# Kernel tuning notes

Measured on AMD Instinct MI355X. Metric: run time of the kernel, lower is better.

## Reference

```python
import jax, jax.numpy as jnp
import numpy as np

B, T, IN_DIM, HID, OUT_DIM = 64, 1024, 128, 512, 64


def _lstm_layer(x, w_ih, w_hh, b_ih, b_hh):
    """Single LSTM layer, batch_first input x: [B, T, D] -> h_seq [B, T, H].
    PyTorch gate order: i, f, g, o. h0 = c0 = 0."""
    H = w_hh.shape[1]
    # Precompute input contribution for all timesteps (one big GEMM).
    xW = jnp.einsum('btd,gd->btg', x, w_ih) + b_ih + b_hh  # [B, T, 4H]
    xW_t = jnp.swapaxes(xW, 0, 1)  # [T, B, 4H] for scan over time

    def step(carry, xw_t):
        h, c = carry
        gates = xw_t + h @ w_hh.T  # [B, 4H]
        i = jax.nn.sigmoid(gates[:, 0 * H:1 * H])
        f = jax.nn.sigmoid(gates[:, 1 * H:2 * H])
        g = jnp.tanh(gates[:, 2 * H:3 * H])
        o = jax.nn.sigmoid(gates[:, 3 * H:4 * H])
        c_new = f * c + i * g
        h_new = o * jnp.tanh(c_new)
        return (h_new, c_new), h_new

    h0 = jnp.zeros((x.shape[0], H), dtype=x.dtype)
    c0 = jnp.zeros((x.shape[0], H), dtype=x.dtype)
    _, h_seq = jax.lax.scan(step, (h0, c0), xW_t)  # h_seq: [T, B, H]
    return jnp.swapaxes(h_seq, 0, 1)  # [B, T, H]


def setup_inputs() -> dict:
    key = jax.random.key(0)
    ks = jax.random.split(key, 12)
    s0 = 1.0 / np.sqrt(HID)  # PyTorch default uniform(-1/sqrt(H), 1/sqrt(H))
    u = lambda k, shape: jax.random.uniform(k, shape, jnp.float32, -s0, s0)
    return {
        'inputs': jax.random.normal(ks[0], (B, T, IN_DIM), jnp.float32),
        # layer 0
        'w_ih_0': u(ks[1], (4 * HID, IN_DIM)),
        'w_hh_0': u(ks[2], (4 * HID, HID)),
        'b_ih_0': u(ks[3], (4 * HID,)),
        'b_hh_0': u(ks[4], (4 * HID,)),
        # layer 1
        'w_ih_1': u(ks[5], (4 * HID, HID)),
        'w_hh_1': u(ks[6], (4 * HID, HID)),
        'b_ih_1': u(ks[7], (4 * HID,)),
        'b_hh_1': u(ks[8], (4 * HID,)),
        # final linear
        'fc_w': u(ks[9], (OUT_DIM, HID)),
        'fc_b': u(ks[10], (OUT_DIM,)),
    }


def reference(inputs, w_ih_0, w_hh_0, b_ih_0, b_hh_0,
              w_ih_1, w_hh_1, b_ih_1, b_hh_1, fc_w, fc_b):
    h1 = _lstm_layer(inputs, w_ih_0, w_hh_0, b_ih_0, b_hh_0)  # [B, T, H]
    h2 = _lstm_layer(h1, w_ih_1, w_hh_1, b_ih_1, b_hh_1)      # [B, T, H]
    last = h2[:, -1, :]                                        # [B, H]
    return last @ fc_w.T + fc_b                                # [B, OUT_DIM]
```

## Files before the change

kernel.cpp:

```cpp
#include <hip/hip_runtime.h>
#include <hip/hip_bf16.h>


#define NTH 256
#define WPG 64
#define NGRP 4
#define BPG 16
#define UPW 8
#define RPW 32
#define HIDDEN 512
#define TSTEPS 1024
#define BATCH 64

#define SPIN_LIMIT 400000000ull

using bf16 = __hip_bfloat16;

__device__ __forceinline__ float b2fl(unsigned short s) {
  return __uint_as_float(((unsigned int)s) << 16);
}

template<typename T> struct Ld4;
template<> struct Ld4<float> {
  static __device__ __forceinline__ float4 go(const float* p) { return *(const float4*)p; }
};
template<> struct Ld4<bf16> {
  static __device__ __forceinline__ float4 go(const bf16* p) {
    ushort4 v = *(const ushort4*)p;
    return make_float4(b2fl(v.x), b2fl(v.y), b2fl(v.z), b2fl(v.w));
  }
};

template<typename T> __device__ __forceinline__ T to_xout(float f);
template<> __device__ __forceinline__ float to_xout<float>(float f) { return f; }
template<> __device__ __forceinline__ bf16 to_xout<bf16>(float f) { return __float2bfloat16(f); }

__device__ __forceinline__ float sigm(float x) { return 1.0f / (1.0f + __expf(-x)); }
__device__ __forceinline__ float tanh_fast(float x) {
  float ax = fabsf(x);
  float e2 = __expf(2.0f * ax);
  float t  = 1.0f - 2.0f / (e2 + 1.0f);
  return copysignf(t, x);
}
__device__ __forceinline__ void fma4(float& a, const float4 w, const float4 h) {
  a = fmaf(w.x, h.x, a);
  a = fmaf(w.y, h.y, a);
  a = fmaf(w.z, h.z, a);
  a = fmaf(w.w, h.w, a);
}

__device__ __forceinline__ void st_cc(float* p, float v) {
  __hip_atomic_store(p, v, __ATOMIC_RELAXED, __HIP_MEMORY_SCOPE_AGENT);
}
__device__ __forceinline__ float ld_cc(const float* p) {
  return __hip_atomic_load((float*)p, __ATOMIC_RELAXED, __HIP_MEMORY_SCOPE_AGENT);
}
__device__ __forceinline__ void cfence() { asm volatile("" ::: "memory"); }

template<int D_IN, bool WRITE_SEQ, typename XIN, typename XOUT>
__global__ __launch_bounds__(NTH, 1)
void lstm_scan(const XIN* __restrict__ xin,
               const float* __restrict__ w_ih,
               const float* __restrict__ w_hh,
               const float* __restrict__ b_ih,
               const float* __restrict__ b_hh,
               float* __restrict__ hbuf,
               XOUT* __restrict__ seqout,
               int* __restrict__ barbase)
{
  constexpr int D4 = D_IN / 4;
  constexpr bool XW_LDS = (D_IN <= 128);
  constexpr int S4 = 128 + (XW_LDS ? D4 : 0);
  constexpr int XC = D_IN / 8;
  constexpr int LD4 = (D_IN == 128) ? 5 : 7;
  constexpr int XPT = (BPG * D4) / NTH;
  constexpr int HPT = (BPG * HIDDEN) / NTH;

  extern __shared__ float lds[];
  float4* wv4 = (float4*)lds;
  float4* hs4 = wv4 + RPW * S4;
  float4* xs4 = hs4 + BPG * 128;
  float*  red = (float*)(xs4 + BPG * D4);
  float*  bsum = red + 8 * 512;
  float*  cst  = bsum + RPW;

  const int tid = threadIdx.x;
  const int bid = blockIdx.x;
  const int g   = bid & 3;
  const int w   = bid >> 2;
  const int b0g = g * BPG;
  const int u0  = w * UPW;
  int* flags = barbase + g * 64;
  int* epoch = barbase + 320 + g * 16;

  for (int idx = tid; idx < RPW * S4; idx += NTH) {
    int r  = idx / S4;
    int c4 = idx - r * S4;
    int swz = (r >> 2) & 7;
    int grow = ((r >> 3) * HIDDEN) + u0 + (r & 7);
    if (c4 < 128) {
      float4 v = *(const float4*)(w_hh + (size_t)grow * HIDDEN + c4 * 4);
      wv4[r * S4 + (c4 ^ swz)] = v;
    } else {
      int c4x = c4 - 128;
      float4 v = *(const float4*)(w_ih + (size_t)grow * D_IN + c4x * 4);
      wv4[r * S4 + 128 + (c4x ^ swz)] = v;
    }
  }
  if (tid < RPW) {
    int grow = ((tid >> 3) * HIDDEN) + u0 + (tid & 7);
    bsum[tid] = b_ih[grow] + b_hh[grow];
  }
  if (tid < UPW * BPG) cst[tid] = 0.0f;

  const int rr = tid & 7;
  const int bb = (tid >> 3) & 3;
  const int kc = tid >> 5;

  const float* wxg[4];
  if (!XW_LDS) {
#pragma unroll
    for (int j = 0; j < 4; ++j) {
      int r = 4 * rr + j;
      int grow = ((r >> 3) * HIDDEN) + u0 + (r & 7);
      wxg[j] = w_ih + (size_t)grow * D_IN;
    }
  }
  __syncthreads();

  for (int t = 0; t < TSTEPS; ++t) {
    const float* hsrc = hbuf + (size_t)(t & 1) * (BATCH * HIDDEN);
    float*       hdst = hbuf + (size_t)((t + 1) & 1) * (BATCH * HIDDEN);

    float4 xr[XPT];
#pragma unroll
    for (int n = 0; n < XPT; ++n) {
      int idx = tid + n * NTH;
      int b = idx >> LD4, c4 = idx & (D4 - 1);
      xr[n] = Ld4<XIN>::go(xin + ((size_t)(b0g + b) * TSTEPS + t) * D_IN + c4 * 4);
    }

    if (t > 0) {
      unsigned long long sp0 = __builtin_amdgcn_s_memrealtime();
      while (__hip_atomic_load(epoch, __ATOMIC_RELAXED, __HIP_MEMORY_SCOPE_AGENT) < t) {
        if (__builtin_amdgcn_s_memrealtime() - sp0 > SPIN_LIMIT) break;
        __builtin_amdgcn_s_sleep(1);
      }
      cfence();
    }

    float hr[HPT];
#pragma unroll
    for (int n = 0; n < HPT; ++n) {
      int idx = tid + n * NTH;
      int b = idx >> 9, c = idx & 511;
      hr[n] = ld_cc(hsrc + (size_t)(b0g + b) * HIDDEN + c);
    }

#pragma unroll
    for (int n = 0; n < XPT; ++n) {
      int idx = tid + n * NTH;
      int b = idx >> LD4, c4 = idx & (D4 - 1);
      xs4[b * D4 + (c4 ^ (b >> 2))] = xr[n];
    }
    __syncthreads();

    float acc[4][4];
#pragma unroll
    for (int j = 0; j < 4; ++j)
#pragma unroll
      for (int i = 0; i < 4; ++i) acc[j][i] = 0.0f;

#pragma unroll 2
    for (int kk = 0; kk < XC / 4; ++kk) {
      const int k4 = kc * (XC / 4) + kk;
      float4 wq[4], xq[4];
      if constexpr (XW_LDS) {
#pragma unroll
        for (int j = 0; j < 4; ++j) wq[j] = wv4[(4 * rr + j) * S4 + 128 + (k4 ^ rr)];
      } else {
#pragma unroll
        for (int j = 0; j < 4; ++j) wq[j] = *(const float4*)(wxg[j] + k4 * 4);
      }
#pragma unroll
      for (int i = 0; i < 4; ++i) xq[i] = xs4[(4 * bb + i) * D4 + (k4 ^ bb)];
#pragma unroll
      for (int j = 0; j < 4; ++j)
#pragma unroll
        for (int i = 0; i < 4; ++i) fma4(acc[j][i], wq[j], xq[i]);
    }

#pragma unroll
    for (int n = 0; n < HPT; ++n) {
      int idx = tid + n * NTH;
      int b = idx >> 9, c = idx & 511;
      ((float*)hs4)[b * 512 + ((((c >> 2) ^ (b >> 2)) << 2) | (c & 3))] = hr[n];
    }
    __syncthreads();

#pragma unroll 4
    for (int kk = 0; kk < 16; ++kk) {
      const int k4 = kc * 16 + kk;
      float4 wq[4], hq[4];
#pragma unroll
      for (int j = 0; j < 4; ++j) wq[j] = wv4[(4 * rr + j) * S4 + (k4 ^ rr)];
#pragma unroll
      for (int i = 0; i < 4; ++i) hq[i] = hs4[(4 * bb + i) * 128 + (k4 ^ bb)];
#pragma unroll
      for (int j = 0; j < 4; ++j)
#pragma unroll
        for (int i = 0; i < 4; ++i) fma4(acc[j][i], wq[j], hq[i]);
    }

#pragma unroll
    for (int j = 0; j < 4; ++j)
#pragma unroll
      for (int i = 0; i < 4; ++i)
        red[kc * 512 + (4 * rr + j) * 16 + 4 * bb + i] = acc[j][i];
    __syncthreads();
    {
      const int a0 = tid, a1 = tid + 256;
      float s0 = bsum[a0 >> 4], s1 = bsum[a1 >> 4];
#pragma unroll
      for (int k2 = 0; k2 < 8; ++k2) {
        s0 += red[k2 * 512 + a0];
        s1 += red[k2 * 512 + a1];
      }
      red[a0] = s0;
      red[a1] = s1;
    }
    __syncthreads();

    if (tid < UPW * BPG) {
      const int lu = tid & 7, bl = tid >> 3;
      float gi = red[(0  + lu) * 16 + bl];
      float gf = red[(8  + lu) * 16 + bl];
      float gg = red[(16 + lu) * 16 + bl];
      float go = red[(24 + lu) * 16 + bl];
      float iv = sigm(gi), fv = sigm(gf), gv = tanh_fast(gg), ov = sigm(go);
      float c = fv * cst[tid] + iv * gv;
      cst[tid] = c;
      float hn = ov * tanh_fast(c);
      const int b = b0g + bl, u = u0 + lu;
      st_cc(hdst + (size_t)b * HIDDEN + u, hn);
      if constexpr (WRITE_SEQ)
        seqout[((size_t)b * TSTEPS + t) * HIDDEN + u] = to_xout<XOUT>(hn);
    }

    __syncthreads();
    if (tid == 0) {
      __hip_atomic_store(&flags[w], t + 1, __ATOMIC_RELAXED, __HIP_MEMORY_SCOPE_AGENT);
    }
    cfence();
    if (w == 0 && tid < WPG) {
      unsigned long long sp0 = __builtin_amdgcn_s_memrealtime();
      while (true) {
        int v = __hip_atomic_load(&flags[tid], __ATOMIC_RELAXED, __HIP_MEMORY_SCOPE_AGENT);
        if (__all(v >= t + 1)) break;
        if (__builtin_amdgcn_s_memrealtime() - sp0 > SPIN_LIMIT) break;
        __builtin_amdgcn_s_sleep(1);
      }
      if (tid == 0)
        __hip_atomic_store(epoch, t + 1, __ATOMIC_RELAXED, __HIP_MEMORY_SCOPE_AGENT);
    }
  }
}

__global__ __launch_bounds__(NTH, 1)
void fc_kernel(const float* __restrict__ h2, const float* __restrict__ fcw,
               const float* __restrict__ fcb, float* __restrict__ out)
{
  extern __shared__ float lds[];
  float4* fw4 = (float4*)lds;
  float4* h24 = fw4 + 64 * 128;
  const int tid = threadIdx.x;
  const int bq  = blockIdx.x;

  for (int idx = tid; idx < 64 * 128; idx += NTH) {
    int o = idx >> 7, c4 = idx & 127;
    fw4[o * 128 + (c4 ^ (o & 7))] = *(const float4*)(fcw + (size_t)o * HIDDEN + c4 * 4);
  }
  for (int idx = tid; idx < 8 * 128; idx += NTH) {
    int b = idx >> 7, c4 = idx & 127;
    h24[b * 128 + c4] = *(const float4*)(h2 + (size_t)(bq * 8 + b) * HIDDEN + c4 * 4);
  }
  __syncthreads();

  const int o = tid & 63, bs = tid >> 6;
  float a0 = 0.f, a1 = 0.f;
  for (int c4 = 0; c4 < 128; ++c4) {
    float4 wv = fw4[o * 128 + (c4 ^ (o & 7))];
    float4 h0 = h24[(2 * bs) * 128 + c4];
    float4 h1 = h24[(2 * bs + 1) * 128 + c4];
    fma4(a0, wv, h0);
    fma4(a1, wv, h1);
  }
  const float bo = fcb[o];
  out[(size_t)(bq * 8 + 2 * bs) * 64 + o]     = a0 + bo;
  out[(size_t)(bq * 8 + 2 * bs + 1) * 64 + o] = a1 + bo;
}

__global__ void init_ws(float* hbuf0, float* hbuf1, int* bars)
{
  int i = blockIdx.x * blockDim.x + threadIdx.x;
  if (i < 2 * BATCH * HIDDEN) { hbuf0[i] = 0.f; hbuf1[i] = 0.f; }
  if (i < 1024) bars[i] = 0;
}

extern "C" void kernel_launch(void* const* d_in, const int* in_sizes, int n_in,
                              void* d_out, int out_size, void* d_ws, size_t ws_size,
                              hipStream_t stream)
{
  const float* x    = (const float*)d_in[0];
  const float* wih0 = (const float*)d_in[1];
  const float* whh0 = (const float*)d_in[2];
  const float* bih0 = (const float*)d_in[3];
  const float* bhh0 = (const float*)d_in[4];
  const float* wih1 = (const float*)d_in[5];
  const float* whh1 = (const float*)d_in[6];
  const float* bih1 = (const float*)d_in[7];
  const float* bhh1 = (const float*)d_in[8];
  const float* fcw  = (const float*)d_in[9];
  const float* fcb  = (const float*)d_in[10];
  float* out = (float*)d_out;

  float* wsf   = (float*)d_ws;
  int*   bars  = (int*)d_ws;
  float* hbuf0 = wsf + 1024;
  float* hbuf1 = hbuf0 + 2 * BATCH * HIDDEN;
  float* seqf  = hbuf1 + 2 * BATCH * HIDDEN;
  const size_t seq_elems = (size_t)BATCH * TSTEPS * HIDDEN;
  const size_t base_bytes = (1024 + 4 * BATCH * HIDDEN) * 4;
  const bool f32seq = ws_size >= base_bytes + seq_elems * 4;

  const size_t lds0  = (size_t)((RPW * 160 + BPG * 128 + BPG * 32) * 4 + 8 * 512 + RPW + 128) * 4;
  const size_t lds1  = (size_t)((RPW * 128 + BPG * 128 + BPG * 128) * 4 + 8 * 512 + RPW + 128) * 4;
  const size_t ldsfc = (size_t)(64 * 128 + 8 * 128) * 16;

  hipLaunchKernelGGL(init_ws, dim3(256), dim3(256), 0, stream, hbuf0, hbuf1, bars);

  int* bar0 = bars;
  int* bar1 = bars + 512;
  float* dummy = nullptr;

  if (f32seq) {
    auto* k0 = lstm_scan<128, true,  float, float>;
    auto* k1 = lstm_scan<512, false, float, float>;
    hipFuncSetAttribute((const void*)k0, hipFuncAttributeMaxDynamicSharedMemorySize, (int)lds0);
    hipFuncSetAttribute((const void*)k1, hipFuncAttributeMaxDynamicSharedMemorySize, (int)lds1);
    float* seqp = seqf;
    void* a0[] = { (void*)&x,    (void*)&wih0, (void*)&whh0, (void*)&bih0, (void*)&bhh0,
                   (void*)&hbuf0, (void*)&seqp, (void*)&bar0 };
    if (hipLaunchCooperativeKernel((const void*)k0, dim3(NGRP * WPG), dim3(NTH), a0,
                                   (unsigned)lds0, stream) != hipSuccess) {
      lstm_scan<128, true, float, float><<<dim3(NGRP * WPG), dim3(NTH), lds0, stream>>>(
          x, wih0, whh0, bih0, bhh0, hbuf0, seqp, bar0);
    }
    const float* seqc = seqf;
    void* a1[] = { (void*)&seqc, (void*)&wih1, (void*)&whh1, (void*)&bih1, (void*)&bhh1,
                   (void*)&hbuf1, (void*)&dummy, (void*)&bar1 };
    if (hipLaunchCooperativeKernel((const void*)k1, dim3(NGRP * WPG), dim3(NTH), a1,
                                   (unsigned)lds1, stream) != hipSuccess) {
      lstm_scan<512, false, float, float><<<dim3(NGRP * WPG), dim3(NTH), lds1, stream>>>(
          seqc, wih1, whh1, bih1, bhh1, hbuf1, dummy, bar1);
    }
  } else {
    auto* k0 = lstm_scan<128, true,  float, bf16>;
    auto* k1 = lstm_scan<512, false, bf16, float>;
    hipFuncSetAttribute((const void*)k0, hipFuncAttributeMaxDynamicSharedMemorySize, (int)lds0);
    hipFuncSetAttribute((const void*)k1, hipFuncAttributeMaxDynamicSharedMemorySize, (int)lds1);
    bf16* seqb = (bf16*)seqf;
    void* a0[] = { (void*)&x,    (void*)&wih0, (void*)&whh0, (void*)&bih0, (void*)&bhh0,
                   (void*)&hbuf0, (void*)&seqb, (void*)&bar0 };
    if (hipLaunchCooperativeKernel((const void*)k0, dim3(NGRP * WPG), dim3(NTH), a0,
                                   (unsigned)lds0, stream) != hipSuccess) {
      lstm_scan<128, true, float, bf16><<<dim3(NGRP * WPG), dim3(NTH), lds0, stream>>>(
          x, wih0, whh0, bih0, bhh0, hbuf0, seqb, bar0);
    }
    const bf16* seqc = (const bf16*)seqf;
    void* a1[] = { (void*)&seqc, (void*)&wih1, (void*)&whh1, (void*)&bih1, (void*)&bhh1,
                   (void*)&hbuf1, (void*)&dummy, (void*)&bar1 };
    if (hipLaunchCooperativeKernel((const void*)k1, dim3(NGRP * WPG), dim3(NTH), a1,
                                   (unsigned)lds1, stream) != hipSuccess) {
      lstm_scan<512, false, bf16, float><<<dim3(NGRP * WPG), dim3(NTH), lds1, stream>>>(
          seqc, wih1, whh1, bih1, bhh1, hbuf1, dummy, bar1);
    }
  }

  hipFuncSetAttribute((const void*)fc_kernel, hipFuncAttributeMaxDynamicSharedMemorySize, (int)ldsfc);
  hipLaunchKernelGGL(fc_kernel, dim3(8), dim3(NTH), ldsfc, stream, hbuf1, fcw, fcb, out);
}
```

Before: 19.51 ms.

## Fuse both LSTM layers into one persistent kernel with wavefront pipelining

Replaces the two sequential per-layer scan launches with one cooperative kernel of 256 blocks. Blocks are split across layer and batch-chunk: layer-1 blocks trail layer-0 through epoch flags, so the two layers run concurrently instead of back to back. Each block alternates between two 16-row batch chunks, so loading one chunk's h/x overlaps the other chunk's compute. The cost is less batch per block, more barrier traffic per step, and cross-layer spin-waits on the sequence buffer.

```diff
diff --git a/kernel.cpp b/kernel.cpp
--- a/kernel.cpp
+++ b/kernel.cpp
@@ -3,11 +3,7 @@
 
 
 #define NTH 256
-#define WPG 64
-#define NGRP 4
 #define BPG 16
-#define UPW 8
-#define RPW 32
 #define HIDDEN 512
 #define TSTEPS 1024
 #define BATCH 64
@@ -19,22 +15,6 @@
 __device__ __forceinline__ float b2fl(unsigned short s) {
   return __uint_as_float(((unsigned int)s) << 16);
 }
-
-template<typename T> struct Ld4;
-template<> struct Ld4<float> {
-  static __device__ __forceinline__ float4 go(const float* p) { return *(const float4*)p; }
-};
-template<> struct Ld4<bf16> {
-  static __device__ __forceinline__ float4 go(const bf16* p) {
-    ushort4 v = *(const ushort4*)p;
-    return make_float4(b2fl(v.x), b2fl(v.y), b2fl(v.z), b2fl(v.w));
-  }
-};
-
-template<typename T> __device__ __forceinline__ T to_xout(float f);
-template<> __device__ __forceinline__ float to_xout<float>(float f) { return f; }
-template<> __device__ __forceinline__ bf16 to_xout<bf16>(float f) { return __float2bfloat16(f); }
-
 __device__ __forceinline__ float sigm(float x) { return 1.0f / (1.0f + __expf(-x)); }
 __device__ __forceinline__ float tanh_fast(float x) {
   float ax = fabsf(x);
@@ -55,163 +35,235 @@
 __device__ __forceinline__ float ld_cc(const float* p) {
   return __hip_atomic_load((float*)p, __ATOMIC_RELAXED, __HIP_MEMORY_SCOPE_AGENT);
 }
+__device__ __forceinline__ void st_cu(unsigned* p, unsigned v) {
+  __hip_atomic_store(p, v, __ATOMIC_RELAXED, __HIP_MEMORY_SCOPE_AGENT);
+}
+__device__ __forceinline__ unsigned ld_cu(const unsigned* p) {
+  return __hip_atomic_load((unsigned*)p, __ATOMIC_RELAXED, __HIP_MEMORY_SCOPE_AGENT);
+}
+__device__ __forceinline__ void st_ci(int* p, int v) {
+  __hip_atomic_store(p, v, __ATOMIC_RELAXED, __HIP_MEMORY_SCOPE_AGENT);
+}
+__device__ __forceinline__ int ld_ci(const int* p) {
+  return __hip_atomic_load((int*)p, __ATOMIC_RELAXED, __HIP_MEMORY_SCOPE_AGENT);
+}
 __device__ __forceinline__ void cfence() { asm volatile("" ::: "memory"); }
 
-template<int D_IN, bool WRITE_SEQ, typename XIN, typename XOUT>
+template<int SEQMODE>
 __global__ __launch_bounds__(NTH, 1)
-void lstm_scan(const XIN* __restrict__ xin,
-               const float* __restrict__ w_ih,
-               const float* __restrict__ w_hh,
-               const float* __restrict__ b_ih,
-               const float* __restrict__ b_hh,
-               float* __restrict__ hbuf,
-               XOUT* __restrict__ seqout,
-               int* __restrict__ barbase)
+void lstm_fused(const float* __restrict__ xin,
+                const float* __restrict__ wih0, const float* __restrict__ whh0,
+                const float* __restrict__ bih0, const float* __restrict__ bhh0,
+                const float* __restrict__ wih1, const float* __restrict__ whh1,
+                const float* __restrict__ bih1, const float* __restrict__ bhh1,
+                float* __restrict__ hbufs,
+                void* __restrict__ seqv,
+                float* __restrict__ fin,
+                int* __restrict__ bars)
 {
-  constexpr int D4 = D_IN / 4;
-  constexpr bool XW_LDS = (D_IN <= 128);
-  constexpr int S4 = 128 + (XW_LDS ? D4 : 0);
-  constexpr int XC = D_IN / 8;
-  constexpr int LD4 = (D_IN == 128) ? 5 : 7;
-  constexpr int XPT = (BPG * D4) / NTH;
-  constexpr int HPT = (BPG * HIDDEN) / NTH;
-
-  extern __shared__ float lds[];
-  float4* wv4 = (float4*)lds;
-  float4* hs4 = wv4 + RPW * S4;
-  float4* xs4 = hs4 + BPG * 128;
-  float*  red = (float*)(xs4 + BPG * D4);
-  float*  bsum = red + 8 * 512;
-  float*  cst  = bsum + RPW;
-
   const int tid = threadIdx.x;
   const int bid = blockIdx.x;
-  const int g   = bid & 3;
-  const int w   = bid >> 2;
-  const int b0g = g * BPG;
-  const int u0  = w * UPW;
-  int* flags = barbase + g * 64;
-  int* epoch = barbase + 320 + g * 16;
-
-  for (int idx = tid; idx < RPW * S4; idx += NTH) {
-    int r  = idx / S4;
-    int c4 = idx - r * S4;
-    int swz = (r >> 2) & 7;
-    int grow = ((r >> 3) * HIDDEN) + u0 + (r & 7);
-    if (c4 < 128) {
-      float4 v = *(const float4*)(w_hh + (size_t)grow * HIDDEN + c4 * 4);
-      wv4[r * S4 + (c4 ^ swz)] = v;
-    } else {
-      int c4x = c4 - 128;
-      float4 v = *(const float4*)(w_ih + (size_t)grow * D_IN + c4x * 4);
-      wv4[r * S4 + 128 + (c4x ^ swz)] = v;
-    }
-  }
-  if (tid < RPW) {
-    int grow = ((tid >> 3) * HIDDEN) + u0 + (tid & 7);
+  const int L   = bid >> 7;
+  const int s   = (bid >> 6) & 1;
+  const int w   = bid & 63;
+  const int u0  = w * 8;
+
+  const float* w_ih = L ? wih1 : wih0;
+  const float* w_hh = L ? whh1 : whh0;
+  const float* b_ih = L ? bih1 : bih0;
+  const float* b_hh = L ? bhh1 : bhh0;
+
+  float*    seqf = (float*)seqv;
+  unsigned* sequ = (unsigned*)seqv;
+
+  extern __shared__ float lds[];
+  float4* wv4  = (float4*)lds;
+  float4* wx4  = wv4 + 32 * 128;
+  float*  st0  = (float*)(wx4 + 32 * 32);
+  float*  st1  = st0 + BPG * HIDDEN;
+  float*  bsum = st1 + BPG * HIDDEN;
+  float*  cst  = bsum + 32;
+  float*  stf[2] = { st0, st1 };
+
+  float* hbc[2]; int* fl[2]; int* ep[2]; int* ep0[2]; int b0c[2];
+#pragma unroll
+  for (int ci = 0; ci < 2; ++ci) {
+    const int c = 2 * s + ci;
+    hbc[ci] = hbufs + (size_t)((L * 4 + c) * 2) * (BPG * HIDDEN);
+    fl[ci]  = bars + (L * 4 + c) * 64;
+    ep[ci]  = bars + 512 + (L * 4 + c) * 16;
+    ep0[ci] = bars + 512 + c * 16;
+    b0c[ci] = c * BPG;
+  }
+
+  for (int idx = tid; idx < 32 * 128; idx += NTH) {
+    int r = idx >> 7, c4 = idx & 127, swz = (r >> 2) & 7;
+    int grow = (r >> 3) * HIDDEN + u0 + (r & 7);
+    wv4[r * 128 + (c4 ^ swz)] = *(const float4*)(w_hh + (size_t)grow * HIDDEN + c4 * 4);
+  }
+  if (L == 0) {
+    for (int idx = tid; idx < 32 * 32; idx += NTH) {
+      int r = idx >> 5, c4 = idx & 31, swz = (r >> 2) & 7;
+      int grow = (r >> 3) * HIDDEN + u0 + (r & 7);
+      wx4[r * 32 + (c4 ^ swz)] = *(const float4*)(w_ih + (size_t)grow * 128 + c4 * 4);
+    }
+  }
+  if (tid < 32) {
+    int grow = (tid >> 3) * HIDDEN + u0 + (tid & 7);
     bsum[tid] = b_ih[grow] + b_hh[grow];
   }
-  if (tid < UPW * BPG) cst[tid] = 0.0f;
+  if (tid < 2 * BPG * 8) cst[tid] = 0.0f;
 
   const int rr = tid & 7;
   const int bb = (tid >> 3) & 3;
   const int kc = tid >> 5;
 
   const float* wxg[4];
-  if (!XW_LDS) {
+  if (L == 1) {
 #pragma unroll
     for (int j = 0; j < 4; ++j) {
       int r = 4 * rr + j;
-      int grow = ((r >> 3) * HIDDEN) + u0 + (r & 7);
-      wxg[j] = w_ih + (size_t)grow * D_IN;
+      int grow = (r >> 3) * HIDDEN + u0 + (r & 7);
+      wxg[j] = w_ih + (size_t)grow * HIDDEN;
     }
   }
   __syncthreads();
 
-  for (int t = 0; t < TSTEPS; ++t) {
-    const float* hsrc = hbuf + (size_t)(t & 1) * (BATCH * HIDDEN);
-    float*       hdst = hbuf + (size_t)((t + 1) & 1) * (BATCH * HIDDEN);
-
-    float4 xr[XPT];
-#pragma unroll
-    for (int n = 0; n < XPT; ++n) {
+  auto waitE = [&](int* e, int tgt) {
+    if (tgt <= 0) return;
+    unsigned long long sp0 = __builtin_amdgcn_s_memrealtime();
+    while (ld_ci(e) < tgt) {
+      if (__builtin_amdgcn_s_memrealtime() - sp0 > SPIN_LIMIT) break;
+      __builtin_amdgcn_s_sleep(1);
+    }
+    cfence();
+  };
+  auto issueH = [&](int ci, int t, float* hr) {
+    const float* hs = hbc[ci] + (size_t)(t & 1) * (BPG * HIDDEN);
+#pragma unroll
+    for (int n = 0; n < 32; ++n) {
       int idx = tid + n * NTH;
-      int b = idx >> LD4, c4 = idx & (D4 - 1);
-      xr[n] = Ld4<XIN>::go(xin + ((size_t)(b0g + b) * TSTEPS + t) * D_IN + c4 * 4);
-    }
-
-    if (t > 0) {
-      unsigned long long sp0 = __builtin_amdgcn_s_memrealtime();
-      while (__hip_atomic_load(epoch, __ATOMIC_RELAXED, __HIP_MEMORY_SCOPE_AGENT) < t) {
-        if (__builtin_amdgcn_s_memrealtime() - sp0 > SPIN_LIMIT) break;
-        __builtin_amdgcn_s_sleep(1);
-      }
-      cfence();
-    }
-
-    float hr[HPT];
-#pragma unroll
-    for (int n = 0; n < HPT; ++n) {
+      int b = idx >> 9, cc = idx & 511;
+      hr[n] = ld_cc(hs + b * 512 + cc);
+    }
+  };
+  auto issueX = [&](int ci, int t, float* xr) {
+    const int b0 = b0c[ci];
+    if (L == 0) {
+#pragma unroll
+      for (int n = 0; n < 2; ++n) {
+        int idx = tid + n * NTH;
+        int b = idx >> 5, c4 = idx & 31;
+        float4 v = *(const float4*)(xin + ((size_t)(b0 + b) * TSTEPS + t) * 128 + c4 * 4);
+        xr[4 * n + 0] = v.x; xr[4 * n + 1] = v.y; xr[4 * n + 2] = v.z; xr[4 * n + 3] = v.w;
+      }
+    } else if (SEQMODE == 0) {
+#pragma unroll
+      for (int n = 0; n < 32; ++n) {
+        int idx = tid + n * NTH;
+        int b = idx >> 9, cc = idx & 511;
+        xr[n] = ld_cc(seqf + ((size_t)(b0 + b) * TSTEPS + t) * HIDDEN + cc);
+      }
+    } else {
+#pragma unroll
+      for (int n = 0; n < 16; ++n) {
+        int idx = tid + n * NTH;
+        int b = idx >> 8, wi = idx & 255;
+        unsigned v = ld_cu(sequ + ((size_t)(b0 + b) * TSTEPS + t) * 256 + wi);
+        xr[2 * n]     = b2fl((unsigned short)(v & 0xffffu));
+        xr[2 * n + 1] = b2fl((unsigned short)(v >> 16));
+      }
+    }
+  };
+  auto stageX = [&](int ci, const float* xr) {
+    float* st = stf[ci];
+    if (L == 0) {
+#pragma unroll
+      for (int n = 0; n < 2; ++n) {
+        int idx = tid + n * NTH;
+        int b = idx >> 5, c4 = idx & 31;
+        ((float4*)st)[b * 32 + (c4 ^ (b >> 2))] =
+            make_float4(xr[4 * n], xr[4 * n + 1], xr[4 * n + 2], xr[4 * n + 3]);
+      }
+    } else if (SEQMODE == 0) {
+#pragma unroll
+      for (int n = 0; n < 32; ++n) {
+        int idx = tid + n * NTH;
+        int b = idx >> 9, cc = idx & 511;
+        st[b * 512 + ((((cc >> 2) ^ (b >> 2)) << 2) | (cc & 3))] = xr[n];
+      }
+    } else {
+#pragma unroll
+      for (int n = 0; n < 16; ++n) {
+        int idx = tid + n * NTH;
+        int b = idx >> 8, wi = idx & 255;
+        int c0 = wi * 2;
+        int base = b * 512 + ((((c0 >> 2) ^ (b >> 2)) << 2) | (c0 & 3));
+        st[base]     = xr[2 * n];
+        st[base + 1] = xr[2 * n + 1];
+      }
+    }
+  };
+  auto stageH = [&](int ci, const float* hr) {
+    float* st = stf[ci];
+#pragma unroll
+    for (int n = 0; n < 32; ++n) {
       int idx = tid + n * NTH;
-      int b = idx >> 9, c = idx & 511;
-      hr[n] = ld_cc(hsrc + (size_t)(b0g + b) * HIDDEN + c);
-    }
-
-#pragma unroll
-    for (int n = 0; n < XPT; ++n) {
-      int idx = tid + n * NTH;
-      int b = idx >> LD4, c4 = idx & (D4 - 1);
-      xs4[b * D4 + (c4 ^ (b >> 2))] = xr[n];
-    }
-    __syncthreads();
-
-    float acc[4][4];
-#pragma unroll
-    for (int j = 0; j < 4; ++j)
-#pragma unroll
-      for (int i = 0; i < 4; ++i) acc[j][i] = 0.0f;
-
+      int b = idx >> 9, cc = idx & 511;
+      st[b * 512 + ((((cc >> 2) ^ (b >> 2)) << 2) | (cc & 3))] = hr[n];
+    }
+  };
+  auto xpart = [&](int ci, float acc[4][4]) {
+    float4* st4 = (float4*)stf[ci];
+    if (L == 0) {
+#pragma unroll
+      for (int kk = 0; kk < 4; ++kk) {
+        const int k4 = kc * 4 + kk;
+        float4 wq[4], xq[4];
+#pragma unroll
+        for (int j = 0; j < 4; ++j) wq[j] = wx4[(4 * rr + j) * 32 + (k4 ^ rr)];
+#pragma unroll
+        for (int i = 0; i < 4; ++i) xq[i] = st4[(4 * bb + i) * 32 + (k4 ^ bb)];
+#pragma unroll
+        for (int j = 0; j < 4; ++j)
+#pragma unroll
+          for (int i = 0; i < 4; ++i) fma4(acc[j][i], wq[j], xq[i]);
+      }
+    } else {
 #pragma unroll 2
-    for (int kk = 0; kk < XC / 4; ++kk) {
-      const int k4 = kc * (XC / 4) + kk;
-      float4 wq[4], xq[4];
-      if constexpr (XW_LDS) {
-#pragma unroll
-        for (int j = 0; j < 4; ++j) wq[j] = wv4[(4 * rr + j) * S4 + 128 + (k4 ^ rr)];
-      } else {
+      for (int kk = 0; kk < 16; ++kk) {
+        const int k4 = kc * 16 + kk;
+        float4 wq[4], xq[4];
 #pragma unroll
         for (int j = 0; j < 4; ++j) wq[j] = *(const float4*)(wxg[j] + k4 * 4);
-      }
-#pragma unroll
-      for (int i = 0; i < 4; ++i) xq[i] = xs4[(4 * bb + i) * D4 + (k4 ^ bb)];
-#pragma unroll
-      for (int j = 0; j < 4; ++j)
-#pragma unroll
-        for (int i = 0; i < 4; ++i) fma4(acc[j][i], wq[j], xq[i]);
-    }
-
-#pragma unroll
-    for (int n = 0; n < HPT; ++n) {
-      int idx = tid + n * NTH;
-      int b = idx >> 9, c = idx & 511;
-      ((float*)hs4)[b * 512 + ((((c >> 2) ^ (b >> 2)) << 2) | (c & 3))] = hr[n];
-    }
-    __syncthreads();
-
+#pragma unroll
+        for (int i = 0; i < 4; ++i) xq[i] = st4[(4 * bb + i) * 128 + (k4 ^ bb)];
+#pragma unroll
+        for (int j = 0; j < 4; ++j)
+#pragma unroll
+          for (int i = 0; i < 4; ++i) fma4(acc[j][i], wq[j], xq[i]);
+      }
+    }
+  };
+  auto hpart = [&](int ci, float acc[4][4]) {
+    float4* st4 = (float4*)stf[ci];
 #pragma unroll 4
     for (int kk = 0; kk < 16; ++kk) {
       const int k4 = kc * 16 + kk;
       float4 wq[4], hq[4];
 #pragma unroll
-      for (int j = 0; j < 4; ++j) wq[j] = wv4[(4 * rr + j) * S4 + (k4 ^ rr)];
-#pragma unroll
-      for (int i = 0; i < 4; ++i) hq[i] = hs4[(4 * bb + i) * 128 + (k4 ^ bb)];
+      for (int j = 0; j < 4; ++j) wq[j] = wv4[(4 * rr + j) * 128 + (k4 ^ rr)];
+#pragma unroll
+      for (int i = 0; i < 4; ++i) hq[i] = st4[(4 * bb + i) * 128 + (k4 ^ bb)];
 #pragma unroll
       for (int j = 0; j < 4; ++j)
 #pragma unroll
         for (int i = 0; i < 4; ++i) fma4(acc[j][i], wq[j], hq[i]);
     }
-
+  };
+  auto finish = [&](int ci, int t, float acc[4][4]) {
+    float* red = stf[ci];
+    __syncthreads();
 #pragma unroll
     for (int j = 0; j < 4; ++j)
 #pragma unroll
@@ -220,49 +272,100 @@
     __syncthreads();
     {
       const int a0 = tid, a1 = tid + 256;
-      float s0 = bsum[a0 >> 4], s1 = bsum[a1 >> 4];
-#pragma unroll
-      for (int k2 = 0; k2 < 8; ++k2) {
-        s0 += red[k2 * 512 + a0];
-        s1 += red[k2 * 512 + a1];
-      }
-      red[a0] = s0;
-      red[a1] = s1;
-    }
-    __syncthreads();
-
-    if (tid < UPW * BPG) {
+      float s0v = bsum[a0 >> 4], s1v = bsum[a1 >> 4];
+#pragma unroll
+      for (int k2 = 0; k2 < 8; ++k2) { s0v += red[k2 * 512 + a0]; s1v += red[k2 * 512 + a1]; }
+      red[a0] = s0v; red[a1] = s1v;
+    }
+    __syncthreads();
+    if (tid < 128) {
       const int lu = tid & 7, bl = tid >> 3;
       float gi = red[(0  + lu) * 16 + bl];
       float gf = red[(8  + lu) * 16 + bl];
       float gg = red[(16 + lu) * 16 + bl];
       float go = red[(24 + lu) * 16 + bl];
       float iv = sigm(gi), fv = sigm(gf), gv = tanh_fast(gg), ov = sigm(go);
-      float c = fv * cst[tid] + iv * gv;
-      cst[tid] = c;
+      float* cc = cst + ci * 128 + tid;
+      float c = fv * (*cc) + iv * gv;
+      *cc = c;
       float hn = ov * tanh_fast(c);
-      const int b = b0g + bl, u = u0 + lu;
-      st_cc(hdst + (size_t)b * HIDDEN + u, hn);
-      if constexpr (WRITE_SEQ)
-        seqout[((size_t)b * TSTEPS + t) * HIDDEN + u] = to_xout<XOUT>(hn);
-    }
-
-    __syncthreads();
-    if (tid == 0) {
-      __hip_atomic_store(&flags[w], t + 1, __ATOMIC_RELAXED, __HIP_MEMORY_SCOPE_AGENT);
-    }
+      st_cc(hbc[ci] + (size_t)((t + 1) & 1) * (BPG * HIDDEN) + bl * 512 + u0 + lu, hn);
+      if (L == 0) {
+        if (SEQMODE == 0) {
+          st_cc(seqf + ((size_t)(b0c[ci] + bl) * TSTEPS + t) * HIDDEN + u0 + lu, hn);
+        } else {
+          float other = __shfl_xor(hn, 1);
+          if ((lu & 1) == 0) {
+            bf16 lo = __float2bfloat16(hn), hi = __float2bfloat16(other);
+            unsigned pv = (unsigned)(*(unsigned short*)&lo) |
+                          ((unsigned)(*(unsigned short*)&hi) << 16);
+            st_cu(sequ + ((size_t)(b0c[ci] + bl) * TSTEPS + t) * 256 + ((u0 + lu) >> 1), pv);
+          }
+        }
+      } else if (t == TSTEPS - 1) {
+        st_cc(fin + (size_t)(b0c[ci] + bl) * HIDDEN + u0 + lu, hn);
+      }
+    }
+    __syncthreads();
+    if (tid == 0) st_ci(fl[ci] + w, t + 1);
     cfence();
-    if (w == 0 && tid < WPG) {
+    if (w == ci && tid < 64) {
       unsigned long long sp0 = __builtin_amdgcn_s_memrealtime();
       while (true) {
-        int v = __hip_atomic_load(&flags[tid], __ATOMIC_RELAXED, __HIP_MEMORY_SCOPE_AGENT);
+        int v = ld_ci(fl[ci] + tid);
         if (__all(v >= t + 1)) break;
         if (__builtin_amdgcn_s_memrealtime() - sp0 > SPIN_LIMIT) break;
         __builtin_amdgcn_s_sleep(1);
       }
-      if (tid == 0)
-        __hip_atomic_store(epoch, t + 1, __ATOMIC_RELAXED, __HIP_MEMORY_SCOPE_AGENT);
-    }
+      if (tid == 0) st_ci(ep[ci], t + 1);
+    }
+  };
+
+  float hrA[32], hrB[32], xrA[32], xrB[32];
+  if (L == 1) waitE(ep0[0], 1);
+  issueX(0, 0, xrA);
+  issueH(0, 0, hrA);
+
+  for (int t = 0; t < TSTEPS; ++t) {
+    float acc[4][4];
+
+    stageX(0, xrA);
+    __syncthreads();
+#pragma unroll
+    for (int j = 0; j < 4; ++j)
+#pragma unroll
+      for (int i = 0; i < 4; ++i) acc[j][i] = 0.0f;
+    xpart(0, acc);
+    {
+      waitE(ep[1], t);
+      if (L == 1) waitE(ep0[1], t + 1);
+      issueX(1, t, xrB);
+      issueH(1, t, hrB);
+    }
+    __syncthreads();
+    stageH(0, hrA);
+    __syncthreads();
+    hpart(0, acc);
+    finish(0, t, acc);
+
+    stageX(1, xrB);
+    __syncthreads();
+#pragma unroll
+    for (int j = 0; j < 4; ++j)
+#pragma unroll
+      for (int i = 0; i < 4; ++i) acc[j][i] = 0.0f;
+    xpart(1, acc);
+    if (t < TSTEPS - 1) {
+      waitE(ep[0], t + 1);
+      if (L == 1) waitE(ep0[0], t + 2);
+      issueX(0, t + 1, xrA);
+      issueH(0, t + 1, hrA);
+    }
+    __syncthreads();
+    stageH(1, hrB);
+    __syncthreads();
+    hpart(1, acc);
+    finish(1, t, acc);
   }
 }
 
@@ -300,10 +403,10 @@
   out[(size_t)(bq * 8 + 2 * bs + 1) * 64 + o] = a1 + bo;
 }
 
-__global__ void init_ws(float* hbuf0, float* hbuf1, int* bars)
+__global__ void init_ws(float* hbufs, int* bars)
 {
   int i = blockIdx.x * blockDim.x + threadIdx.x;
-  if (i < 2 * BATCH * HIDDEN) { hbuf0[i] = 0.f; hbuf1[i] = 0.f; }
+  if (i < 2 * 4 * 2 * BPG * HIDDEN) hbufs[i] = 0.f;
   if (i < 1024) bars[i] = 0;
 }
 
@@ -326,67 +429,46 @@
 
   float* wsf   = (float*)d_ws;
   int*   bars  = (int*)d_ws;
-  float* hbuf0 = wsf + 1024;
-  float* hbuf1 = hbuf0 + 2 * BATCH * HIDDEN;
-  float* seqf  = hbuf1 + 2 * BATCH * HIDDEN;
-  const size_t seq_elems = (size_t)BATCH * TSTEPS * HIDDEN;
-  const size_t base_bytes = (1024 + 4 * BATCH * HIDDEN) * 4;
-  const bool f32seq = ws_size >= base_bytes + seq_elems * 4;
-
-  const size_t lds0  = (size_t)((RPW * 160 + BPG * 128 + BPG * 32) * 4 + 8 * 512 + RPW + 128) * 4;
-  const size_t lds1  = (size_t)((RPW * 128 + BPG * 128 + BPG * 128) * 4 + 8 * 512 + RPW + 128) * 4;
+  float* hbufs = wsf + 1024;
+  float* fin   = hbufs + 2 * 4 * 2 * BPG * HIDDEN;
+  void*  seqv  = (void*)(fin + BATCH * HIDDEN);
+
+  const size_t head_bytes = (size_t)(1024 + 131072 + 32768) * 4;
+  const size_t seq_f32    = (size_t)BATCH * TSTEPS * HIDDEN * 4;
+  const bool f32seq = ws_size >= head_bytes + seq_f32;
+
+  const size_t ldsF  = (size_t)(32 * 128 + 32 * 32) * 16 +
+                       (size_t)(2 * BPG * HIDDEN + 32 + 256) * 4;
   const size_t ldsfc = (size_t)(64 * 128 + 8 * 128) * 16;
 
-  hipLaunchKernelGGL(init_ws, dim3(256), dim3(256), 0, stream, hbuf0, hbuf1, bars);
-
-  int* bar0 = bars;
-  int* bar1 = bars + 512;
-  float* dummy = nullptr;
+  hipLaunchKernelGGL(init_ws, dim3(512), dim3(256), 0, stream, hbufs, bars);
 
   if (f32seq) {
-    auto* k0 = lstm_scan<128, true,  float, float>;
-    auto* k1 = lstm_scan<512, false, float, float>;
-    hipFuncSetAttribute((const void*)k0, hipFuncAttributeMaxDynamicSharedMemorySize, (int)lds0);
-    hipFuncSetAttribute((const void*)k1, hipFuncAttributeMaxDynamicSharedMemorySize, (int)lds1);
-    float* seqp = seqf;
-    void* a0[] = { (void*)&x,    (void*)&wih0, (void*)&whh0, (void*)&bih0, (void*)&bhh0,
-                   (void*)&hbuf0, (void*)&seqp, (void*)&bar0 };
-    if (hipLaunchCooperativeKernel((const void*)k0, dim3(NGRP * WPG), dim3(NTH), a0,
-                                   (unsigned)lds0, stream) != hipSuccess) {
-      lstm_scan<128, true, float, float><<<dim3(NGRP * WPG), dim3(NTH), lds0, stream>>>(
-          x, wih0, whh0, bih0, bhh0, hbuf0, seqp, bar0);
-    }
-    const float* seqc = seqf;
-    void* a1[] = { (void*)&seqc, (void*)&wih1, (void*)&whh1, (void*)&bih1, (void*)&bhh1,
-                   (void*)&hbuf1, (void*)&dummy, (void*)&bar1 };
-    if (hipLaunchCooperativeKernel((const void*)k1, dim3(NGRP * WPG), dim3(NTH), a1,
-                                   (unsigned)lds1, stream) != hipSuccess) {
-      lstm_scan<512, false, float, float><<<dim3(NGRP * WPG), dim3(NTH), lds1, stream>>>(
-          seqc, wih1, whh1, bih1, bhh1, hbuf1, dummy, bar1);
+    auto* k = lstm_fused<0>;
+    hipFuncSetAttribute((const void*)k, hipFuncAttributeMaxDynamicSharedMemorySize, (int)ldsF);
+    void* args[] = { (void*)&x,
+                     (void*)&wih0, (void*)&whh0, (void*)&bih0, (void*)&bhh0,
+                     (void*)&wih1, (void*)&whh1, (void*)&bih1, (void*)&bhh1,
+                     (void*)&hbufs, (void*)&seqv, (void*)&fin, (void*)&bars };
+    if (hipLaunchCooperativeKernel((const void*)k, dim3(256), dim3(NTH), args,
+                                   (unsigned)ldsF, stream) != hipSuccess) {
+      lstm_fused<0><<<dim3(256), dim3(NTH), ldsF, stream>>>(
+          x, wih0, whh0, bih0, bhh0, wih1, whh1, bih1, bhh1, hbufs, seqv, fin, bars);
     }
   } else {
-    auto* k0 = lstm_scan<128, true,  float, bf16>;
-    auto* k1 = lstm_scan<512, false, bf16, float>;
-    hipFuncSetAttribute((const void*)k0, hipFuncAttributeMaxDynamicSharedMemorySize, (int)lds0);
-    hipFuncSetAttribute((const void*)k1, hipFuncAttributeMaxDynamicSharedMemorySize, (int)lds1);
-    bf16* seqb = (bf16*)seqf;
-    void* a0[] = { (void*)&x,    (void*)&wih0, (void*)&whh0, (void*)&bih0, (void*)&bhh0,
-                   (void*)&hbuf0, (void*)&seqb, (void*)&bar0 };
-    if (hipLaunchCooperativeKernel((const void*)k0, dim3(NGRP * WPG), dim3(NTH), a0,
-                                   (unsigned)lds0, stream) != hipSuccess) {
-      lstm_scan<128, true, float, bf16><<<dim3(NGRP * WPG), dim3(NTH), lds0, stream>>>(
-          x, wih0, whh0, bih0, bhh0, hbuf0, seqb, bar0);
-    }
-    const bf16* seqc = (const bf16*)seqf;
-    void* a1[] = { (void*)&seqc, (void*)&wih1, (void*)&whh1, (void*)&bih1, (void*)&bhh1,
-                   (void*)&hbuf1, (void*)&dummy, (void*)&bar1 };
-    if (hipLaunchCooperativeKernel((const void*)k1, dim3(NGRP * WPG), dim3(NTH), a1,
-                                   (unsigned)lds1, stream) != hipSuccess) {
-      lstm_scan<512, false, bf16, float><<<dim3(NGRP * WPG), dim3(NTH), lds1, stream>>>(
-          seqc, wih1, whh1, bih1, bhh1, hbuf1, dummy, bar1);
+    auto* k = lstm_fused<1>;
+    hipFuncSetAttribute((const void*)k, hipFuncAttributeMaxDynamicSharedMemorySize, (int)ldsF);
+    void* args[] = { (void*)&x,
+                     (void*)&wih0, (void*)&whh0, (void*)&bih0, (void*)&bhh0,
+                     (void*)&wih1, (void*)&whh1, (void*)&bih1, (void*)&bhh1,
+                     (void*)&hbufs, (void*)&seqv, (void*)&fin, (void*)&bars };
+    if (hipLaunchCooperativeKernel((const void*)k, dim3(256), dim3(NTH), args,
+                                   (unsigned)ldsF, stream) != hipSuccess) {
+      lstm_fused<1><<<dim3(256), dim3(NTH), ldsF, stream>>>(
+          x, wih0, whh0, bih0, bhh0, wih1, whh1, bih1, bhh1, hbufs, seqv, fin, bars);
     }
   }
 
   hipFuncSetAttribute((const void*)fc_kernel, hipFuncAttributeMaxDynamicSharedMemorySize, (int)ldsfc);
-  hipLaunchKernelGGL(fc_kernel, dim3(8), dim3(NTH), ldsfc, stream, hbuf1, fcw, fcb, out);
-}
+  hipLaunchKernelGGL(fc_kernel, dim3(8), dim3(NTH), ldsfc, stream, fin, fcw, fcb, out);
+}
```

After: 32.78 ms. 68.0% more time.

## Overlap input projection with barrier wait and vectorize h loads

Applied to the files above, without the earlier changes.

Moves the wait on the group epoch barrier after the x·W_ih partial product, so the input contribution is computed while other blocks finish the previous step. The per-step h reload becomes eight coherent dwordx4 loads in inline asm instead of scalar atomic loads. The per-wait spin timeout is replaced with a single kernel-wide deadline. The risk is that the inline asm with a full waitcnt and sched barrier limits compiler scheduling, and the global deadline changes timeout semantics.

```diff
diff --git a/kernel.cpp b/kernel.cpp
--- a/kernel.cpp
+++ b/kernel.cpp
@@ -12,7 +12,7 @@
 #define TSTEPS 1024
 #define BATCH 64
 
-#define SPIN_LIMIT 400000000ull
+#define SPIN_BUDGET 400000000ull
 
 using bf16 = __hip_bfloat16;
 
@@ -52,10 +52,39 @@
 __device__ __forceinline__ void st_cc(float* p, float v) {
   __hip_atomic_store(p, v, __ATOMIC_RELAXED, __HIP_MEMORY_SCOPE_AGENT);
 }
-__device__ __forceinline__ float ld_cc(const float* p) {
-  return __hip_atomic_load((float*)p, __ATOMIC_RELAXED, __HIP_MEMORY_SCOPE_AGENT);
+__device__ __forceinline__ void st_ci(int* p, int v) {
+  __hip_atomic_store(p, v, __ATOMIC_RELAXED, __HIP_MEMORY_SCOPE_AGENT);
+}
+__device__ __forceinline__ int ld_ci(const int* p) {
+  return __hip_atomic_load((int*)p, __ATOMIC_RELAXED, __HIP_MEMORY_SCOPE_AGENT);
 }
 __device__ __forceinline__ void cfence() { asm volatile("" ::: "memory"); }
+
+__device__ __forceinline__ void ld_h8(const float4* base, int tid, float4 hv[8]) {
+  const float4* p0 = base + tid;
+  const float4* p1 = base + tid + 1 * NTH;
+  const float4* p2 = base + tid + 2 * NTH;
+  const float4* p3 = base + tid + 3 * NTH;
+  const float4* p4 = base + tid + 4 * NTH;
+  const float4* p5 = base + tid + 5 * NTH;
+  const float4* p6 = base + tid + 6 * NTH;
+  const float4* p7 = base + tid + 7 * NTH;
+  asm volatile(
+      "global_load_dwordx4 %0, %8, off sc0 sc1\n\t"
+      "global_load_dwordx4 %1, %9, off sc0 sc1\n\t"
+      "global_load_dwordx4 %2, %10, off sc0 sc1\n\t"
+      "global_load_dwordx4 %3, %11, off sc0 sc1\n\t"
+      "global_load_dwordx4 %4, %12, off sc0 sc1\n\t"
+      "global_load_dwordx4 %5, %13, off sc0 sc1\n\t"
+      "global_load_dwordx4 %6, %14, off sc0 sc1\n\t"
+      "global_load_dwordx4 %7, %15, off sc0 sc1\n\t"
+      "s_waitcnt vmcnt(0)"
+      : "=&v"(hv[0]), "=&v"(hv[1]), "=&v"(hv[2]), "=&v"(hv[3]),
+        "=&v"(hv[4]), "=&v"(hv[5]), "=&v"(hv[6]), "=&v"(hv[7])
+      : "v"(p0), "v"(p1), "v"(p2), "v"(p3), "v"(p4), "v"(p5), "v"(p6), "v"(p7)
+      : "memory");
+  __builtin_amdgcn_sched_barrier(0);
+}
 
 template<int D_IN, bool WRITE_SEQ, typename XIN, typename XOUT>
 __global__ __launch_bounds__(NTH, 1)
@@ -74,7 +103,6 @@
   constexpr int XC = D_IN / 8;
   constexpr int LD4 = (D_IN == 128) ? 5 : 7;
   constexpr int XPT = (BPG * D4) / NTH;
-  constexpr int HPT = (BPG * HIDDEN) / NTH;
 
   extern __shared__ float lds[];
   float4* wv4 = (float4*)lds;
@@ -92,6 +120,9 @@
   const int u0  = w * UPW;
   int* flags = barbase + g * 64;
   int* epoch = barbase + 320 + g * 16;
+
+  const unsigned long long deadline =
+      __builtin_amdgcn_s_memrealtime() + SPIN_BUDGET;
 
   for (int idx = tid; idx < RPW * S4; idx += NTH) {
     int r  = idx / S4;
@@ -132,36 +163,12 @@
     const float* hsrc = hbuf + (size_t)(t & 1) * (BATCH * HIDDEN);
     float*       hdst = hbuf + (size_t)((t + 1) & 1) * (BATCH * HIDDEN);
 
-    float4 xr[XPT];
 #pragma unroll
     for (int n = 0; n < XPT; ++n) {
       int idx = tid + n * NTH;
       int b = idx >> LD4, c4 = idx & (D4 - 1);
-      xr[n] = Ld4<XIN>::go(xin + ((size_t)(b0g + b) * TSTEPS + t) * D_IN + c4 * 4);
-    }
-
-    if (t > 0) {
-      unsigned long long sp0 = __builtin_amdgcn_s_memrealtime();
-      while (__hip_atomic_load(epoch, __ATOMIC_RELAXED, __HIP_MEMORY_SCOPE_AGENT) < t) {
-        if (__builtin_amdgcn_s_memrealtime() - sp0 > SPIN_LIMIT) break;
-        __builtin_amdgcn_s_sleep(1);
-      }
-      cfence();
-    }
-
-    float hr[HPT];
-#pragma unroll
-    for (int n = 0; n < HPT; ++n) {
-      int idx = tid + n * NTH;
-      int b = idx >> 9, c = idx & 511;
-      hr[n] = ld_cc(hsrc + (size_t)(b0g + b) * HIDDEN + c);
-    }
-
-#pragma unroll
-    for (int n = 0; n < XPT; ++n) {
-      int idx = tid + n * NTH;
-      int b = idx >> LD4, c4 = idx & (D4 - 1);
-      xs4[b * D4 + (c4 ^ (b >> 2))] = xr[n];
+      float4 v = Ld4<XIN>::go(xin + ((size_t)(b0g + b) * TSTEPS + t) * D_IN + c4 * 4);
+      xs4[b * D4 + (c4 ^ (b >> 2))] = v;
     }
     __syncthreads();
 
@@ -190,11 +197,23 @@
         for (int i = 0; i < 4; ++i) fma4(acc[j][i], wq[j], xq[i]);
     }
 
-#pragma unroll
-    for (int n = 0; n < HPT; ++n) {
-      int idx = tid + n * NTH;
-      int b = idx >> 9, c = idx & 511;
-      ((float*)hs4)[b * 512 + ((((c >> 2) ^ (b >> 2)) << 2) | (c & 3))] = hr[n];
+    if (t > 0) {
+      while (ld_ci(epoch) < t) {
+        if (__builtin_amdgcn_s_memrealtime() > deadline) break;
+        __builtin_amdgcn_s_sleep(1);
+      }
+      cfence();
+    }
+
+    {
+      float4 hv[8];
+      ld_h8((const float4*)(hsrc + (size_t)b0g * HIDDEN), tid, hv);
+#pragma unroll
+      for (int n = 0; n < 8; ++n) {
+        int idx = tid + n * NTH;
+        int b = idx >> 7, c4 = idx & 127;
+        hs4[b * 128 + (c4 ^ (b >> 2))] = hv[n];
+      }
     }
     __syncthreads();
 
@@ -248,20 +267,17 @@
     }
 
     __syncthreads();
-    if (tid == 0) {
-      __hip_atomic_store(&flags[w], t + 1, __ATOMIC_RELAXED, __HIP_MEMORY_SCOPE_AGENT);
-    }
+    if (tid == 0)
+      st_ci(&flags[w], t + 1);
     cfence();
     if (w == 0 && tid < WPG) {
-      unsigned long long sp0 = __builtin_amdgcn_s_memrealtime();
       while (true) {
-        int v = __hip_atomic_load(&flags[tid], __ATOMIC_RELAXED, __HIP_MEMORY_SCOPE_AGENT);
+        int v = ld_ci(&flags[tid]);
         if (__all(v >= t + 1)) break;
-        if (__builtin_amdgcn_s_memrealtime() - sp0 > SPIN_LIMIT) break;
+        if (__builtin_amdgcn_s_memrealtime() > deadline) break;
         __builtin_amdgcn_s_sleep(1);
       }
-      if (tid == 0)
-        __hip_atomic_store(epoch, t + 1, __ATOMIC_RELAXED, __HIP_MEMORY_SCOPE_AGENT);
+      if (tid == 0) st_ci(epoch, t + 1);
     }
   }
 }
```

Result: faster. 18.54 ms (-5.0%).
